# Optimization experiments

Hardware: AMD Instinct MI355X
Metric: run time of the kernel (lower is better)

## Reference

```python
import jax, jax.numpy as jnp
import numpy as np
from itertools import permutations

BLOCK = 64  # GroupLinear block_size


def _dist_bucket_table():
    # replicates self.distance: log2-style bucketing of token distances [0,1024)
    t = np.zeros(1024, dtype=np.int32)
    for i, th in enumerate([2, 4, 8, 16, 32, 64, 128, 256, 512]):
        t[th:] = i + 1
    return jnp.asarray(t)


def setup_inputs() -> dict:
    key = jax.random.key(0)
    ks = jax.random.split(key, 12)
    B, S, H, NH = 4, 512, 768, 12
    E, TAG, TE, TD, R = 24, 7, 20, 20, 97
    DIN = 2 * H + TE + TD
    hidden_state = jax.random.normal(ks[0], (B, S, H), jnp.float32)
    attention = jax.random.uniform(ks[1], (B, NH, S, S), jnp.float32)
    attention_mask = jnp.ones((B, S), jnp.float32)
    head = jnp.sort(jax.random.randint(ks[2], (B, E), 0, S), axis=-1)
    tail = jnp.sort(jax.random.randint(ks[3], (B, E), 0, S), axis=-1)
    entity_type = jax.random.randint(ks[4], (B, E), 0, TAG)
    type_table = jax.random.normal(ks[5], (TAG, TE), jnp.float32) * 0.02
    dis_table = jax.random.normal(ks[6], (20, TD), jnp.float32) * 0.02
    Wh = jax.random.normal(ks[7], (DIN, H), jnp.float32) * (1.0 / np.sqrt(DIN))
    bh = jnp.zeros((H,), jnp.float32)
    Wt = jax.random.normal(ks[8], (DIN, H), jnp.float32) * (1.0 / np.sqrt(DIN))
    bt = jnp.zeros((H,), jnp.float32)
    # GroupLinear weight reshaped to [n_blocks, BLOCK, BLOCK, R]
    clsW = jax.random.normal(ks[9], (H // BLOCK, BLOCK, BLOCK, R), jnp.float32) * (1.0 / np.sqrt(H * BLOCK))
    clsb = jnp.zeros((R,), jnp.float32)
    return dict(hidden_state=hidden_state, attention=attention,
                attention_mask=attention_mask, head=head, tail=tail,
                entity_type=entity_type, type_table=type_table,
                dis_table=dis_table, Wh=Wh, bh=bh, Wt=Wt, bt=bt,
                clsW=clsW, clsb=clsb)


def reference(hidden_state, attention, attention_mask, head, tail, entity_type,
              type_table, dis_table, Wh, bh, Wt, bt, clsW, clsb):
    E = head.shape[1]
    hts = jnp.asarray(list(permutations(range(E), 2)), dtype=jnp.int32)  # [P,2]
    i0, i1 = hts[:, 0], hts[:, 1]
    dtab = _dist_bucket_table()
    att = attention.sum(axis=1)  # [B,S,S] sum over heads

    def per_sample(h, a, m, hd, tl, et):
        # h:[S,H] a:[S,S] m:[S] hd,tl,et:[E]
        ent_feat = (h[hd] + h[tl]) * 0.5          # [E,H]
        ent_att = (a[hd] + a[tl]) * 0.5           # [E,S]
        ent_tf = type_table[et]                   # [E,TE]
        head_f, tail_f = ent_feat[i0], ent_feat[i1]      # [P,H]
        ht_att = ent_att[i0] * ent_att[i1] * m[None, :]  # [P,S]
        head_ty, tail_ty = ent_tf[i0], ent_tf[i1]        # [P,TE]
        d = dtab[jnp.abs(tl[i0] - hd[i1])]               # [P]
        ht_dist = dis_table[d]                           # [P,TD]
        ht_att = ht_att / (ht_att.sum(-1, keepdims=True) + 1e-20)
        ht_info = ht_att @ h                             # [P,H]
        all_h = jnp.concatenate([head_f, ht_info, head_ty, ht_dist], axis=-1)
        all_t = jnp.concatenate([tail_f, ht_info, tail_ty, ht_dist], axis=-1)
        return all_h, all_t

    all_h, all_t = jax.vmap(per_sample)(hidden_state, att, attention_mask,
                                        head, tail, entity_type)
    all_h = all_h.reshape(-1, all_h.shape[-1])  # [B*P, DIN]
    all_t = all_t.reshape(-1, all_t.shape[-1])
    h1 = jnp.tanh(all_h @ Wh + bh)              # [L,H]
    t1 = jnp.tanh(all_t @ Wt + bt)
    L, H = h1.shape
    nb = H // BLOCK
    x1 = h1.reshape(L, nb, BLOCK)
    x2 = t1.reshape(L, nb, BLOCK)
    # GroupLinear: per-block outer product then linear, fused as einsum
    logits = jnp.einsum('lnb,lnc,nbcr->lr', x1, x2, clsW) + clsb  # [L,R]
    return logits
```

## Files before the change

### kernel.cpp

```cpp
#include <hip/hip_runtime.h>
#include <hip/hip_bf16.h>
#include <math.h>

#define B_ 4
#define S_ 512
#define H_ 768
#define NH_ 12
#define E_ 24
#define TE_ 20
#define TD_ 20
#define R_ 97
#define DIN_ 1576
#define KPAD_ 1600
#define KS_MLP 50
#define MF_MLP 140
#define KS_HTI 16
#define P_ 552
#define L_ 2208
#define NB_ 12
#define NF_ 7

typedef __bf16 bf16x8 __attribute__((ext_vector_type(8)));
typedef float f32x4 __attribute__((ext_vector_type(4)));

__device__ __forceinline__ unsigned short f2bf(float f) {
  union { float f; unsigned u; } c; c.f = f;
  unsigned r = c.u + 0x7FFF + ((c.u >> 16) & 1);
  return (unsigned short)(r >> 16);
}
__device__ __forceinline__ float bf2f(unsigned short b) {
  union { unsigned u; float f; } c; c.u = ((unsigned)b) << 16;
  return c.f;
}
__device__ __forceinline__ unsigned pk2(float a, float b) {
  return (unsigned)f2bf(a) | ((unsigned)f2bf(b) << 16);
}
__device__ __forceinline__ void gload_lds16(const uint4* g, uint4* l) {
  __builtin_amdgcn_global_load_lds(
      (const __attribute__((address_space(1))) unsigned*)(const void*)g,
      (__attribute__((address_space(3))) unsigned*)(void*)l, 16, 0, 0);
}

__global__ void ent_prep(const float* __restrict__ attn, const float* __restrict__ hs,
                         const int* __restrict__ head, const int* __restrict__ tail,
                         float* __restrict__ ent_att, float* __restrict__ ent_feat) {
  int be = blockIdx.x;
  int b = be / E_;
  int hd = head[be], tl = tail[be];
  int tid = threadIdx.x;
  const float* abase = attn + (size_t)b * NH_ * S_ * S_;
  for (int s = tid; s < S_; s += 256) {
    float acc = 0.f;
#pragma unroll
    for (int nh = 0; nh < NH_; ++nh) {
      const float* ap = abase + (size_t)nh * S_ * S_;
      acc += ap[(size_t)hd * S_ + s] + ap[(size_t)tl * S_ + s];
    }
    ent_att[(size_t)be * S_ + s] = 0.5f * acc;
  }
  const float* hb = hs + (size_t)b * S_ * H_;
  for (int k = tid; k < H_; k += 256) {
    ent_feat[(size_t)be * H_ + k] = 0.5f * (hb[(size_t)hd * H_ + k] + hb[(size_t)tl * H_ + k]);
  }
}

__global__ void pair_att(const float* __restrict__ ent_att, const float* __restrict__ mask,
                         const int* __restrict__ head, const int* __restrict__ tail,
                         const int* __restrict__ etype,
                         float* __restrict__ ht_att, int* __restrict__ meta) {
  int l = blockIdx.x;
  int b = l / P_, p = l % P_;
  int i0 = p / (E_ - 1), rem = p % (E_ - 1);
  int i1 = rem + (rem >= i0 ? 1 : 0);
  int tid = threadIdx.x;
  if (tid == 0) {
    meta[0 * L_ + l] = b * E_ + i0;
    meta[1 * L_ + l] = b * E_ + i1;
    meta[2 * L_ + l] = etype[b * E_ + i0];
    meta[3 * L_ + l] = etype[b * E_ + i1];
    int d = abs(tail[b * E_ + i0] - head[b * E_ + i1]);
    int bk = (d >= 2) + (d >= 4) + (d >= 8) + (d >= 16) + (d >= 32) +
             (d >= 64) + (d >= 128) + (d >= 256) + (d >= 512);
    meta[4 * L_ + l] = bk;
  }
  const float* a0 = ent_att + (size_t)(b * E_ + i0) * S_;
  const float* a1 = ent_att + (size_t)(b * E_ + i1) * S_;
  const float* m = mask + (size_t)b * S_;
  float v0 = a0[tid] * a1[tid] * m[tid];
  float v1 = a0[tid + 256] * a1[tid + 256] * m[tid + 256];
  float loc = v0 + v1;
  for (int o = 32; o > 0; o >>= 1) loc += __shfl_down(loc, o, 64);
  __shared__ float red[4];
  if ((tid & 63) == 0) red[tid >> 6] = loc;
  __syncthreads();
  float tot = red[0] + red[1] + red[2] + red[3];
  float inv = 1.f / (tot + 1e-20f);
  ht_att[(size_t)l * S_ + tid] = v0 * inv;
  ht_att[(size_t)l * S_ + tid + 256] = v1 * inv;
}

__global__ void pack_hs(const float* __restrict__ hs, uint4* __restrict__ hsP) {
  int u = blockIdx.x * 256 + threadIdx.x;
  if (u >= B_ * KS_HTI * 48 * 64) return;
  int lane = u & 63;
  int t = u >> 6;
  int nt16 = t % 48;
  int t2 = t / 48;
  int ks = t2 % KS_HTI;
  int b = t2 / KS_HTI;
  int n = nt16 * 16 + (lane & 15);
  int k0 = ks * 32 + ((lane >> 4) << 3);
  const float* src = hs + (size_t)b * S_ * H_;
  unsigned w[4];
#pragma unroll
  for (int q = 0; q < 4; ++q) {
    int k = k0 + 2 * q;
    w[q] = pk2(src[(size_t)k * H_ + n], src[(size_t)(k + 1) * H_ + n]);
  }
  uint4 o; o.x = w[0]; o.y = w[1]; o.z = w[2]; o.w = w[3];
  hsP[u] = o;
}

__global__ void pack_Wmlp(const float* __restrict__ Wh, const float* __restrict__ Wt,
                          uint4* __restrict__ WpH, uint4* __restrict__ WpT) {
  int u = blockIdx.x * 256 + threadIdx.x;
  if (u >= KS_MLP * 48 * 64) return;
  const float* W = blockIdx.y ? Wt : Wh;
  uint4* Wp = blockIdx.y ? WpT : WpH;
  int lane = u & 63;
  int t = u >> 6;
  int nt16 = t % 48;
  int ks = t / 48;
  int n = nt16 * 16 + (lane & 15);
  int k0 = ks * 32 + ((lane >> 4) << 3);
  unsigned w[4];
#pragma unroll
  for (int q = 0; q < 4; ++q) {
    int k = k0 + 2 * q;
    float v0 = (k < DIN_) ? W[(size_t)k * H_ + n] : 0.f;
    float v1 = (k + 1 < DIN_) ? W[(size_t)(k + 1) * H_ + n] : 0.f;
    w[q] = pk2(v0, v1);
  }
  uint4 o; o.x = w[0]; o.y = w[1]; o.z = w[2]; o.w = w[3];
  Wp[u] = o;
}

__global__ void pack_allx(const float* __restrict__ ent_feat, const float* __restrict__ ht_info,
                          const float* __restrict__ ttab, const float* __restrict__ dtab,
                          const int* __restrict__ meta,
                          uint4* __restrict__ axH, uint4* __restrict__ axT) {
  int idx = blockIdx.x * 256 + threadIdx.x;
  int lane = idx & 63;
  int unit = idx >> 6;
  int half = unit / (MF_MLP * KS_MLP);
  int rem = unit % (MF_MLP * KS_MLP);
  int mf = rem / KS_MLP, ks = rem % KS_MLP;
  int row = mf * 16 + (lane & 15);
  int k = ks * 32 + ((lane >> 4) << 3);
  uint4 d; d.x = d.y = d.z = d.w = 0;
  if (row < L_) {
    int frow = meta[half * L_ + row];
    int trow = meta[(2 + half) * L_ + row];
    int db = meta[4 * L_ + row];
    if (k < 768) {
      const float* p = ent_feat + (size_t)frow * H_ + k;
      float4 v0 = *(const float4*)p, v1 = *(const float4*)(p + 4);
      d.x = pk2(v0.x, v0.y); d.y = pk2(v0.z, v0.w);
      d.z = pk2(v1.x, v1.y); d.w = pk2(v1.z, v1.w);
    } else if (k < 1536) {
      const float* p = ht_info + (size_t)row * H_ + (k - 768);
      float4 v0 = *(const float4*)p, v1 = *(const float4*)(p + 4);
      d.x = pk2(v0.x, v0.y); d.y = pk2(v0.z, v0.w);
      d.z = pk2(v1.x, v1.y); d.w = pk2(v1.z, v1.w);
    } else {
      float v[8];
#pragma unroll
      for (int j = 0; j < 8; ++j) {
        int e = k + j;
        v[j] = (e < 1556) ? ttab[trow * TE_ + (e - 1536)]
             : (e < 1576) ? dtab[db * TD_ + (e - 1556)] : 0.f;
      }
      d.x = pk2(v[0], v[1]); d.y = pk2(v[2], v[3]);
      d.z = pk2(v[4], v[5]); d.w = pk2(v[6], v[7]);
    }
  }
  (half ? axT : axH)[(size_t)rem * 64 + lane] = d;
}

__global__ __launch_bounds__(256) void htinfo_mfma(
    const float* __restrict__ htatt, const uint4* __restrict__ hsP,
    float* __restrict__ htinfo) {
  int b = blockIdx.z;
  int m0 = blockIdx.x * 64;
  int nt0 = blockIdx.y * 4;
  int tid = threadIdx.x;
  int wave = tid >> 6, lane = tid & 63;
  int wm = wave & 1, wn = wave >> 1;
  __shared__ __align__(16) uint4 Ash[2][512];
  __shared__ __align__(16) uint4 Bsh[2][512];

  f32x4 acc[2][2];
#pragma unroll
  for (int i = 0; i < 2; ++i)
#pragma unroll
    for (int j = 0; j < 2; ++j) acc[i][j] = (f32x4){0.f, 0.f, 0.f, 0.f};

  auto stageB = [&](int s, int buf) {
#pragma unroll
    for (int i = 0; i < 2; ++i) {
      int c = wave * 2 + i;
      int ntl = c >> 1, kslot = c & 1;
      gload_lds16(hsP + ((size_t)(b * KS_HTI + s * 2 + kslot) * 48 + nt0 + ntl) * 64 + lane,
                  &Bsh[buf][c * 64]);
    }
  };
  auto gatherA = [&](int s, int c, uint4& d) {
    int mfl = c >> 1, kslot = c & 1;
    int row = m0 + mfl * 16 + (lane & 15);
    if (row >= P_) { d.x = d.y = d.z = d.w = 0; return; }
    int k = s * 64 + kslot * 32 + ((lane >> 4) << 3);
    const float* p = htatt + ((size_t)b * P_ + row) * S_ + k;
    float4 v0 = *(const float4*)p, v1 = *(const float4*)(p + 4);
    d.x = pk2(v0.x, v0.y); d.y = pk2(v0.z, v0.w);
    d.z = pk2(v1.x, v1.y); d.w = pk2(v1.z, v1.w);
  };

  {
    uint4 a0_, a1_;
    gatherA(0, wave, a0_); gatherA(0, wave + 4, a1_);
    Ash[0][wave * 64 + lane] = a0_;
    Ash[0][(wave + 4) * 64 + lane] = a1_;
    stageB(0, 0);
  }
  __syncthreads();

  for (int s = 0; s < 8; ++s) {
    int cur = s & 1, nxt = cur ^ 1;
    bool more = (s + 1 < 8);
    uint4 aN0, aN1;
    if (more) {
      stageB(s + 1, nxt);
      gatherA(s + 1, wave, aN0); gatherA(s + 1, wave + 4, aN1);
    }
    bf16x8 af[2][2], bf[2][2];
#pragma unroll
    for (int mf = 0; mf < 2; ++mf)
#pragma unroll
      for (int kc = 0; kc < 2; ++kc)
        af[mf][kc] = *(const bf16x8*)&Ash[cur][((wm * 2 + mf) * 2 + kc) * 64 + lane];
#pragma unroll
    for (int nf = 0; nf < 2; ++nf)
#pragma unroll
      for (int kc = 0; kc < 2; ++kc)
        bf[nf][kc] = *(const bf16x8*)&Bsh[cur][((wn * 2 + nf) * 2 + kc) * 64 + lane];
#pragma unroll
    for (int kc = 0; kc < 2; ++kc)
#pragma unroll
      for (int nf = 0; nf < 2; ++nf)
#pragma unroll
        for (int mf = 0; mf < 2; ++mf)
          acc[mf][nf] = __builtin_amdgcn_mfma_f32_16x16x32_bf16(af[mf][kc], bf[nf][kc], acc[mf][nf], 0, 0, 0);
    if (more) {
      Ash[nxt][wave * 64 + lane] = aN0;
      Ash[nxt][(wave + 4) * 64 + lane] = aN1;
    }
    __syncthreads();
  }

#pragma unroll
  for (int mf = 0; mf < 2; ++mf)
#pragma unroll
    for (int nf = 0; nf < 2; ++nf) {
      int n = nt0 * 16 + (wn * 2 + nf) * 16 + (lane & 15);
#pragma unroll
      for (int reg = 0; reg < 4; ++reg) {
        int l = m0 + (wm * 2 + mf) * 16 + ((lane >> 4) << 2) + reg;
        if (l < P_)
          htinfo[((size_t)b * P_ + l) * H_ + n] = acc[mf][nf][reg];
      }
    }
}

__global__ __launch_bounds__(256) void mlp_mfma(
    const uint4* __restrict__ Apk_h, const uint4* __restrict__ Apk_t,
    const uint4* __restrict__ Wp_h, const uint4* __restrict__ Wp_t,
    const float* __restrict__ bh, const float* __restrict__ bt,
    float* __restrict__ h1, float* __restrict__ t1) {
  int half = blockIdx.z;
  const uint4* Apk = half ? Apk_t : Apk_h;
  const uint4* Wp = half ? Wp_t : Wp_h;
  const float* bias = half ? bt : bh;
  float* out = half ? t1 : h1;
  int mf0 = blockIdx.x * 4;
  int nt0 = blockIdx.y * 4;
  int tid = threadIdx.x;
  int wave = tid >> 6, lane = tid & 63;
  int wm = wave & 1, wn = wave >> 1;
  __shared__ __align__(16) uint4 Ash[2][512];
  __shared__ __align__(16) uint4 Bsh[2][512];

  f32x4 acc[2][2];
#pragma unroll
  for (int i = 0; i < 2; ++i)
#pragma unroll
    for (int j = 0; j < 2; ++j) acc[i][j] = (f32x4){0.f, 0.f, 0.f, 0.f};

  auto stage = [&](int s, int buf) {
#pragma unroll
    for (int i = 0; i < 2; ++i) {
      int c = wave * 2 + i;
      int cl = c >> 1, kslot = c & 1;
      gload_lds16(Apk + ((size_t)(mf0 + cl) * KS_MLP + s * 2 + kslot) * 64 + lane,
                  &Ash[buf][c * 64]);
      gload_lds16(Wp + ((size_t)(s * 2 + kslot) * 48 + nt0 + cl) * 64 + lane,
                  &Bsh[buf][c * 64]);
    }
  };

  stage(0, 0);
  __syncthreads();

  for (int s = 0; s < 25; ++s) {
    int cur = s & 1, nxt = cur ^ 1;
    if (s + 1 < 25) stage(s + 1, nxt);
    bf16x8 af[2][2], bf[2][2];
#pragma unroll
    for (int mf = 0; mf < 2; ++mf)
#pragma unroll
      for (int kc = 0; kc < 2; ++kc)
        af[mf][kc] = *(const bf16x8*)&Ash[cur][((wm * 2 + mf) * 2 + kc) * 64 + lane];
#pragma unroll
    for (int nf = 0; nf < 2; ++nf)
#pragma unroll
      for (int kc = 0; kc < 2; ++kc)
        bf[nf][kc] = *(const bf16x8*)&Bsh[cur][((wn * 2 + nf) * 2 + kc) * 64 + lane];
#pragma unroll
    for (int kc = 0; kc < 2; ++kc)
#pragma unroll
      for (int nf = 0; nf < 2; ++nf)
#pragma unroll
        for (int mf = 0; mf < 2; ++mf)
          acc[mf][nf] = __builtin_amdgcn_mfma_f32_16x16x32_bf16(af[mf][kc], bf[nf][kc], acc[mf][nf], 0, 0, 0);
    __syncthreads();
  }

#pragma unroll
  for (int mf = 0; mf < 2; ++mf)
#pragma unroll
    for (int nf = 0; nf < 2; ++nf) {
      int n = nt0 * 16 + (wn * 2 + nf) * 16 + (lane & 15);
      float bv = bias[n];
#pragma unroll
      for (int reg = 0; reg < 4; ++reg) {
        int l = (mf0 + wm * 2 + mf) * 16 + ((lane >> 4) << 2) + reg;
        if (l < L_)
          out[(size_t)l * H_ + n] = tanhf(acc[mf][nf][reg] + bv);
      }
    }
}

__global__ void pack_w(const float* __restrict__ clsW, uint4* __restrict__ Wfrag) {
  int nb = blockIdx.x;
  __shared__ float Wls[64][98];
  int tid = threadIdx.x;
  const float* src = clsW + (size_t)nb * 64 * R_;
  for (int idx = tid; idx < 64 * R_; idx += 256) {
    Wls[idx / R_][idx % R_] = src[idx];
  }
  __syncthreads();
  for (int u = tid; u < 896; u += 256) {
    int nf = u >> 7;
    int kc = (u >> 6) & 1;
    int lane = u & 63;
    int r = (lane & 15) + 16 * nf;
    unsigned w[4];
#pragma unroll
    for (int q = 0; q < 4; ++q) {
      int c0 = ((lane >> 4) << 3) + 2 * q + 32 * kc;
      float v0 = (r < R_) ? Wls[c0][r] : 0.f;
      float v1 = (r < R_) ? Wls[c0 + 1][r] : 0.f;
      w[q] = (unsigned)f2bf(v0) | ((unsigned)f2bf(v1) << 16);
    }
    uint4 o; o.x = w[0]; o.y = w[1]; o.z = w[2]; o.w = w[3];
    Wfrag[(size_t)nb * 896 + u] = o;
  }
}

__global__ __launch_bounds__(256) void bilinear_mfma(
    const float* __restrict__ h1, const float* __restrict__ t1,
    const uint4* __restrict__ Wfrag, float* __restrict__ part,
    float* __restrict__ part2) {
  int blk = blockIdx.x;
  int xcd = blk & 7;
  int slot = blk >> 3;
  int pg = slot / 36;
  int j = slot % 36;
  int p = pg * 8 + xcd;
  int n = p >> 1, z = p & 1;
  int l0 = j * 64;
  int tid = threadIdx.x;
  int wave = tid >> 6, lane = tid & 63;
  int wm = wave & 1, kh = wave >> 1;
  __shared__ unsigned short x1s[32][66];
  __shared__ float red[128 * 56];

  for (int i = tid; i < 512; i += 256) {
    int row = i >> 3, cq = (i & 7) * 4;
    float4 v = make_float4(0, 0, 0, 0);
    if (l0 + row < L_)
      v = *(const float4*)(h1 + (size_t)(l0 + row) * H_ + n * 64 + z * 32 + cq);
    x1s[cq + 0][row] = f2bf(v.x);
    x1s[cq + 1][row] = f2bf(v.y);
    x1s[cq + 2][row] = f2bf(v.z);
    x1s[cq + 3][row] = f2bf(v.w);
  }

  float x2f[2][2][8];
#pragma unroll
  for (int mf = 0; mf < 2; ++mf) {
    int row = l0 + wm * 32 + mf * 16 + (lane & 15);
#pragma unroll
    for (int kc = 0; kc < 2; ++kc) {
      float4 v0 = make_float4(0, 0, 0, 0), v1 = v0;
      if (row < L_) {
        const float* ptr = t1 + (size_t)row * H_ + n * 64 + kc * 32 + ((lane >> 4) << 3);
        v0 = *(const float4*)ptr;
        v1 = *(const float4*)(ptr + 4);
      }
      x2f[mf][kc][0] = v0.x; x2f[mf][kc][1] = v0.y;
      x2f[mf][kc][2] = v0.z; x2f[mf][kc][3] = v0.w;
      x2f[mf][kc][4] = v1.x; x2f[mf][kc][5] = v1.y;
      x2f[mf][kc][6] = v1.z; x2f[mf][kc][7] = v1.w;
    }
  }

  f32x4 acc[2][NF_];
#pragma unroll
  for (int mf = 0; mf < 2; ++mf)
#pragma unroll
    for (int nf = 0; nf < NF_; ++nf)
      acc[mf][nf] = (f32x4){0.f, 0.f, 0.f, 0.f};

  __syncthreads();

  const uint4* gbase = Wfrag + (size_t)n * 64 * 896;
  int bbase = z * 32 + kh * 16;
  uint4 wreg[7];
  {
    const uint4* gs = gbase + (size_t)bbase * 896 + lane;
#pragma unroll
    for (int nf = 0; nf < 7; ++nf) wreg[nf] = gs[nf * 128];
  }

#pragma unroll 2
  for (int s = 0; s < 32; ++s) {
    uint4 wnx[7];
    if (s + 1 < 32) {
      int b = bbase + ((s + 1) >> 1);
      int kcn = (s + 1) & 1;
      const uint4* gs = gbase + (size_t)b * 896 + kcn * 64 + lane;
#pragma unroll
      for (int nf = 0; nf < 7; ++nf) wnx[nf] = gs[nf * 128];
    }
    int bl = kh * 16 + (s >> 1);
    int kc = s & 1;
    bf16x8 afr[2];
#pragma unroll
    for (int mf = 0; mf < 2; ++mf) {
      float x1v = bf2f(x1s[bl][wm * 32 + mf * 16 + (lane & 15)]);
#pragma unroll
      for (int jj = 0; jj < 8; ++jj)
        afr[mf][jj] = (__bf16)(x1v * x2f[mf][kc][jj]);
    }
#pragma unroll
    for (int nf = 0; nf < NF_; ++nf) {
      union { uint4 u; bf16x8 b; } cvt;
      cvt.u = wreg[nf];
#pragma unroll
      for (int mf = 0; mf < 2; ++mf)
        acc[mf][nf] = __builtin_amdgcn_mfma_f32_16x16x32_bf16(
            afr[mf], cvt.b, acc[mf][nf], 0, 0, 0);
    }
#pragma unroll
    for (int nf = 0; nf < 7; ++nf) wreg[nf] = wnx[nf];
  }

  int rbase = (wm * 64 + lane) * 56;
  if (kh == 1) {
#pragma unroll
    for (int mf = 0; mf < 2; ++mf)
#pragma unroll
      for (int nf = 0; nf < NF_; ++nf)
        *(f32x4*)&red[rbase + (mf * NF_ + nf) * 4] = acc[mf][nf];
  }
  __syncthreads();
  if (kh == 0) {
    float* dst = (z == 0) ? part : part2;
#pragma unroll
    for (int mf = 0; mf < 2; ++mf) {
#pragma unroll
      for (int nf = 0; nf < NF_; ++nf) {
        acc[mf][nf] += *(const f32x4*)&red[rbase + (mf * NF_ + nf) * 4];
        int r = nf * 16 + (lane & 15);
        if (r < R_) {
#pragma unroll
          for (int reg = 0; reg < 4; ++reg) {
            int l = l0 + wm * 32 + mf * 16 + ((lane >> 4) << 2) + reg;
            if (l < L_)
              dst[((size_t)n * L_ + l) * R_ + r] = acc[mf][nf][reg];
          }
        }
      }
    }
  }
}

__global__ void reduce_logits(const float* __restrict__ part, const float* __restrict__ part2,
                              const float* __restrict__ clsb, float* __restrict__ out) {
  int idx = blockIdx.x * 256 + threadIdx.x;
  if (idx < L_ * R_) {
    int r = idx % R_;
    float s = clsb[r];
#pragma unroll
    for (int nn = 0; nn < NB_; ++nn)
      s += part[(size_t)nn * L_ * R_ + idx] + part2[(size_t)nn * L_ * R_ + idx];
    out[idx] = s;
  }
}

extern "C" void kernel_launch(void* const* d_in, const int* in_sizes, int n_in,
                              void* d_out, int out_size, void* d_ws, size_t ws_size,
                              hipStream_t stream) {
  const float* hs   = (const float*)d_in[0];
  const float* attn = (const float*)d_in[1];
  const float* mask = (const float*)d_in[2];
  const int*   head = (const int*)d_in[3];
  const int*   tail = (const int*)d_in[4];
  const int*   etyp = (const int*)d_in[5];
  const float* ttab = (const float*)d_in[6];
  const float* dtab = (const float*)d_in[7];
  const float* Wh   = (const float*)d_in[8];
  const float* bh   = (const float*)d_in[9];
  const float* Wt   = (const float*)d_in[10];
  const float* bt   = (const float*)d_in[11];
  const float* clsW = (const float*)d_in[12];
  const float* clsb = (const float*)d_in[13];
  float* out = (float*)d_out;

  float* ws = (float*)d_ws;
  float* ent_att  = ws; ws += (size_t)B_ * E_ * S_;
  float* ent_feat = ws; ws += (size_t)B_ * E_ * H_;
  float* ht_att   = ws; ws += (size_t)L_ * S_;
  float* ht_info  = ws; ws += (size_t)L_ * H_;
  float* h1       = ws; ws += (size_t)L_ * H_;
  float* t1       = ws; ws += (size_t)L_ * H_;
  float* part     = ws; ws += (size_t)NB_ * L_ * R_;
  uint4* Wpack_h  = (uint4*)ws; ws += (size_t)KS_MLP * 48 * 64 * 4;
  uint4* Wpack_t  = (uint4*)ws; ws += (size_t)KS_MLP * 48 * 64 * 4;
  uint4* hsPack   = (uint4*)ws; ws += (size_t)B_ * KS_HTI * 48 * 64 * 4;
  uint4* Wfrag    = (uint4*)ws; ws += (size_t)NB_ * 64 * 896 * 4;
  uint4* allx_h   = (uint4*)ws; ws += (size_t)MF_MLP * KS_MLP * 64 * 4;
  uint4* allx_t   = (uint4*)ws; ws += (size_t)MF_MLP * KS_MLP * 64 * 4;
  int* meta = (int*)ws;
  float* part2 = (float*)allx_h;

  ent_prep<<<B_ * E_, 256, 0, stream>>>(attn, hs, head, tail, ent_att, ent_feat);
  pair_att<<<L_, 256, 0, stream>>>(ent_att, mask, head, tail, etyp, ht_att, meta);
  pack_hs<<<(B_ * KS_HTI * 48 * 64) / 256, 256, 0, stream>>>(hs, hsPack);
  htinfo_mfma<<<dim3(9, 12, B_), 256, 0, stream>>>(ht_att, hsPack, ht_info);
  pack_Wmlp<<<dim3((KS_MLP * 48 * 64) / 256, 2), 256, 0, stream>>>(Wh, Wt, Wpack_h, Wpack_t);
  pack_allx<<<(2 * MF_MLP * KS_MLP * 64) / 256, 256, 0, stream>>>(
      ent_feat, ht_info, ttab, dtab, meta, allx_h, allx_t);
  mlp_mfma<<<dim3(35, 12, 2), 256, 0, stream>>>(allx_h, allx_t,
      Wpack_h, Wpack_t, bh, bt, h1, t1);
  pack_w<<<NB_ * 64, 256, 0, stream>>>(clsW, Wfrag);
  bilinear_mfma<<<864, 256, 0, stream>>>(h1, t1, Wfrag, part, part2);
  reduce_logits<<<(L_ * R_ + 255) / 256, 256, 0, stream>>>(part, part2, clsb, out);
}
```

Measured before the change: 126.3 us.

## Give each bilinear block a full 64-row tile and full block depth

The bilinear GroupLinear kernel now assigns each workgroup all 64 b-indices of a block and 64 rows of L, with each wave covering 16 b-values for all 64 rows. Before, the work was split into two z halves, each written to its own partial buffer. Dropping that split halves the grid, removes the second partial buffer, and halves the reads in the final reduce kernel. Each wave now reuses every weight fragment across four M-fragments instead of two. The cost is twice the accumulator registers per wave, a serialized three-step LDS reduction across waves with extra barriers, and fewer blocks in flight.

```diff
diff --git a/kernel.cpp b/kernel.cpp
--- a/kernel.cpp
+++ b/kernel.cpp
@@ -388,37 +388,36 @@
 
 __global__ __launch_bounds__(256) void bilinear_mfma(
     const float* __restrict__ h1, const float* __restrict__ t1,
-    const uint4* __restrict__ Wfrag, float* __restrict__ part,
-    float* __restrict__ part2) {
+    const uint4* __restrict__ Wfrag, float* __restrict__ part) {
   int blk = blockIdx.x;
   int xcd = blk & 7;
   int slot = blk >> 3;
-  int pg = slot / 36;
-  int j = slot % 36;
-  int p = pg * 8 + xcd;
-  int n = p >> 1, z = p & 1;
+  int pg = slot / 18;
+  int jsub = slot % 18;
+  int grp = pg * 8 + xcd;
+  int n = grp >> 1;
+  int j = (grp & 1) * 18 + jsub;
   int l0 = j * 64;
   int tid = threadIdx.x;
   int wave = tid >> 6, lane = tid & 63;
-  int wm = wave & 1, kh = wave >> 1;
-  __shared__ unsigned short x1s[32][66];
-  __shared__ float red[128 * 56];
-
-  for (int i = tid; i < 512; i += 256) {
-    int row = i >> 3, cq = (i & 7) * 4;
+  __shared__ unsigned short x1s[64][66];
+  __shared__ float red[64][114];
+
+  for (int i = tid; i < 1024; i += 256) {
+    int row = i >> 4, bq = (i & 15) * 4;
     float4 v = make_float4(0, 0, 0, 0);
     if (l0 + row < L_)
-      v = *(const float4*)(h1 + (size_t)(l0 + row) * H_ + n * 64 + z * 32 + cq);
-    x1s[cq + 0][row] = f2bf(v.x);
-    x1s[cq + 1][row] = f2bf(v.y);
-    x1s[cq + 2][row] = f2bf(v.z);
-    x1s[cq + 3][row] = f2bf(v.w);
-  }
-
-  float x2f[2][2][8];
-#pragma unroll
-  for (int mf = 0; mf < 2; ++mf) {
-    int row = l0 + wm * 32 + mf * 16 + (lane & 15);
+      v = *(const float4*)(h1 + (size_t)(l0 + row) * H_ + n * 64 + bq);
+    x1s[bq + 0][row] = f2bf(v.x);
+    x1s[bq + 1][row] = f2bf(v.y);
+    x1s[bq + 2][row] = f2bf(v.z);
+    x1s[bq + 3][row] = f2bf(v.w);
+  }
+
+  float x2f[4][2][8];
+#pragma unroll
+  for (int mf = 0; mf < 4; ++mf) {
+    int row = l0 + mf * 16 + (lane & 15);
 #pragma unroll
     for (int kc = 0; kc < 2; ++kc) {
       float4 v0 = make_float4(0, 0, 0, 0), v1 = v0;
@@ -434,9 +433,9 @@
     }
   }
 
-  f32x4 acc[2][NF_];
-#pragma unroll
-  for (int mf = 0; mf < 2; ++mf)
+  f32x4 acc[4][NF_];
+#pragma unroll
+  for (int mf = 0; mf < 4; ++mf)
 #pragma unroll
     for (int nf = 0; nf < NF_; ++nf)
       acc[mf][nf] = (f32x4){0.f, 0.f, 0.f, 0.f};
@@ -444,7 +443,7 @@
   __syncthreads();
 
   const uint4* gbase = Wfrag + (size_t)n * 64 * 896;
-  int bbase = z * 32 + kh * 16;
+  int bbase = wave * 16;
   uint4 wreg[7];
   {
     const uint4* gs = gbase + (size_t)bbase * 896 + lane;
@@ -462,12 +461,12 @@
 #pragma unroll
       for (int nf = 0; nf < 7; ++nf) wnx[nf] = gs[nf * 128];
     }
-    int bl = kh * 16 + (s >> 1);
+    int b = bbase + (s >> 1);
     int kc = s & 1;
-    bf16x8 afr[2];
-#pragma unroll
-    for (int mf = 0; mf < 2; ++mf) {
-      float x1v = bf2f(x1s[bl][wm * 32 + mf * 16 + (lane & 15)]);
+    bf16x8 afr[4];
+#pragma unroll
+    for (int mf = 0; mf < 4; ++mf) {
+      float x1v = bf2f(x1s[b][mf * 16 + (lane & 15)]);
 #pragma unroll
       for (int jj = 0; jj < 8; ++jj)
         afr[mf][jj] = (__bf16)(x1v * x2f[mf][kc][jj]);
@@ -477,7 +476,7 @@
       union { uint4 u; bf16x8 b; } cvt;
       cvt.u = wreg[nf];
 #pragma unroll
-      for (int mf = 0; mf < 2; ++mf)
+      for (int mf = 0; mf < 4; ++mf)
         acc[mf][nf] = __builtin_amdgcn_mfma_f32_16x16x32_bf16(
             afr[mf], cvt.b, acc[mf][nf], 0, 0, 0);
     }
@@ -485,29 +484,36 @@
     for (int nf = 0; nf < 7; ++nf) wreg[nf] = wnx[nf];
   }
 
-  int rbase = (wm * 64 + lane) * 56;
-  if (kh == 1) {
-#pragma unroll
-    for (int mf = 0; mf < 2; ++mf)
-#pragma unroll
-      for (int nf = 0; nf < NF_; ++nf)
-        *(f32x4*)&red[rbase + (mf * NF_ + nf) * 4] = acc[mf][nf];
-  }
-  __syncthreads();
-  if (kh == 0) {
-    float* dst = (z == 0) ? part : part2;
-#pragma unroll
-    for (int mf = 0; mf < 2; ++mf) {
+  for (int w = 1; w < 4; ++w) {
+    if (wave == w) {
+#pragma unroll
+      for (int mf = 0; mf < 4; ++mf)
+#pragma unroll
+        for (int nf = 0; nf < NF_; ++nf)
+          *(f32x4*)&red[lane][(mf * NF_ + nf) * 4] = acc[mf][nf];
+    }
+    __syncthreads();
+    if (wave == 0) {
+#pragma unroll
+      for (int mf = 0; mf < 4; ++mf)
+#pragma unroll
+        for (int nf = 0; nf < NF_; ++nf)
+          acc[mf][nf] += *(const f32x4*)&red[lane][(mf * NF_ + nf) * 4];
+    }
+    __syncthreads();
+  }
+  if (wave == 0) {
+#pragma unroll
+    for (int mf = 0; mf < 4; ++mf) {
 #pragma unroll
       for (int nf = 0; nf < NF_; ++nf) {
-        acc[mf][nf] += *(const f32x4*)&red[rbase + (mf * NF_ + nf) * 4];
         int r = nf * 16 + (lane & 15);
         if (r < R_) {
 #pragma unroll
           for (int reg = 0; reg < 4; ++reg) {
-            int l = l0 + wm * 32 + mf * 16 + ((lane >> 4) << 2) + reg;
+            int l = l0 + mf * 16 + ((lane >> 4) << 2) + reg;
             if (l < L_)
-              dst[((size_t)n * L_ + l) * R_ + r] = acc[mf][nf][reg];
+              part[((size_t)n * L_ + l) * R_ + r] = acc[mf][nf][reg];
           }
         }
       }
@@ -515,15 +521,14 @@
   }
 }
 
-__global__ void reduce_logits(const float* __restrict__ part, const float* __restrict__ part2,
-                              const float* __restrict__ clsb, float* __restrict__ out) {
+__global__ void reduce_logits(const float* __restrict__ part, const float* __restrict__ clsb,
+                              float* __restrict__ out) {
   int idx = blockIdx.x * 256 + threadIdx.x;
   if (idx < L_ * R_) {
     int r = idx % R_;
     float s = clsb[r];
 #pragma unroll
-    for (int nn = 0; nn < NB_; ++nn)
-      s += part[(size_t)nn * L_ * R_ + idx] + part2[(size_t)nn * L_ * R_ + idx];
+    for (int nn = 0; nn < NB_; ++nn) s += part[(size_t)nn * L_ * R_ + idx];
     out[idx] = s;
   }
 }
@@ -562,7 +567,6 @@
   uint4* allx_h   = (uint4*)ws; ws += (size_t)MF_MLP * KS_MLP * 64 * 4;
   uint4* allx_t   = (uint4*)ws; ws += (size_t)MF_MLP * KS_MLP * 64 * 4;
   int* meta = (int*)ws;
-  float* part2 = (float*)allx_h;
 
   ent_prep<<<B_ * E_, 256, 0, stream>>>(attn, hs, head, tail, ent_att, ent_feat);
   pair_att<<<L_, 256, 0, stream>>>(ent_att, mask, head, tail, etyp, ht_att, meta);
@@ -574,6 +578,6 @@
   mlp_mfma<<<dim3(35, 12, 2), 256, 0, stream>>>(allx_h, allx_t,
       Wpack_h, Wpack_t, bh, bt, h1, t1);
   pack_w<<<NB_ * 64, 256, 0, stream>>>(clsW, Wfrag);
-  bilinear_mfma<<<864, 256, 0, stream>>>(h1, t1, Wfrag, part, part2);
-  reduce_logits<<<(L_ * R_ + 255) / 256, 256, 0, stream>>>(part, part2, clsb, out);
-}
+  bilinear_mfma<<<432, 256, 0, stream>>>(h1, t1, Wfrag, part);
+  reduce_logits<<<(L_ * R_ + 255) / 256, 256, 0, stream>>>(part, clsb, out);
+}
```

New measurement: 136.6 us. +8.2%, slower.
